# Optimization experiments

Measured on AMD Instinct MI355X. Metric: run time of the kernel, lower is better.

Reference implementation:

```python
import jax, jax.numpy as jnp
import numpy as np

N = 100000
IN_PLANES = 64
OUT_PLANES = 64
SHARE = 8
NSAMPLE = 16


def setup_inputs() -> dict:
    key = jax.random.key(0)
    ks = jax.random.split(key, 20)
    f32 = jnp.float32
    s = lambda fan_in: 1.0 / np.sqrt(fan_in)
    inp = {}
    inp['p'] = jax.random.normal(ks[0], (N, 3), f32)
    inp['x'] = jax.random.normal(ks[1], (N, IN_PLANES), f32)
    inp['knn_idx'] = jax.random.randint(ks[2], (N, NSAMPLE), 0, N, jnp.int64)
    # channelMixMLPs01: Linear(3+in, nsample) -> ReLU -> Bilinear(ns, ns, ns)
    inp['W01'] = jax.random.uniform(ks[3], (3 + IN_PLANES, NSAMPLE), f32, -s(3 + IN_PLANES), s(3 + IN_PLANES))
    inp['b01'] = jnp.zeros((NSAMPLE,), f32)
    inp['Wbil'] = jax.random.uniform(ks[4], (NSAMPLE, NSAMPLE, NSAMPLE), f32, -s(NSAMPLE), s(NSAMPLE))
    inp['bbil'] = jnp.zeros((NSAMPLE,), f32)
    # linear_p: Linear(3,3) -> BN(3) -> ReLU -> Linear(3, out)
    inp['Wp1'] = jax.random.uniform(ks[5], (3, 3), f32, -s(3), s(3))
    inp['bp1'] = jnp.zeros((3,), f32)
    inp['bnp_s'] = jnp.ones((3,), f32)   # BN folded (inference): scale = gamma/sqrt(var+eps)
    inp['bnp_b'] = jnp.zeros((3,), f32)  # shift = beta - mean*scale
    inp['Wp2'] = jax.random.uniform(ks[6], (3, OUT_PLANES), f32, -s(3), s(3))
    inp['bp2'] = jnp.zeros((OUT_PLANES,), f32)
    # channelMixMLPs02
    mid = OUT_PLANES
    inp['W2a'] = jax.random.uniform(ks[7], (2 * NSAMPLE, mid), f32, -s(2 * NSAMPLE), s(2 * NSAMPLE))
    inp['bn2a_s'] = jnp.ones((mid,), f32)
    inp['bn2a_b'] = jnp.zeros((mid,), f32)
    inp['W2b'] = jax.random.uniform(ks[8], (mid, mid // SHARE), f32, -s(mid), s(mid))
    inp['bn2b_s'] = jnp.ones((mid // SHARE,), f32)
    inp['bn2b_b'] = jnp.zeros((mid // SHARE,), f32)
    inp['W2c'] = jax.random.uniform(ks[9], (mid // SHARE, OUT_PLANES // SHARE), f32, -s(mid // SHARE), s(mid // SHARE))
    inp['b2c'] = jnp.zeros((OUT_PLANES // SHARE,), f32)
    # channelMixMLPs03: Linear(in, out)
    inp['W3'] = jax.random.uniform(ks[10], (IN_PLANES, OUT_PLANES), f32, -s(IN_PLANES), s(IN_PLANES))
    inp['b3'] = jnp.zeros((OUT_PLANES,), f32)
    return inp


def reference(p, x, knn_idx, W01, b01, Wbil, bbil, Wp1, bp1, bnp_s, bnp_b,
              Wp2, bp2, W2a, bn2a_s, bn2a_b, W2b, bn2b_s, bn2b_b, W2c, b2c,
              W3, b3):
    n, k = knn_idx.shape
    out_planes = W3.shape[1]
    share = SHARE
    # queryandgroup(use_xyz=True): gather neighbors, relative xyz concat features
    p_r = p[knn_idx] - p[:, None, :]                      # [n,k,3]
    x_knn_in = jnp.concatenate([p_r, x[knn_idx]], -1)     # [n,k,3+in]
    xf = x_knn_in.reshape(n * k, -1)
    # channelMixMLPs01: Linear -> ReLU -> Bilinear(e, e)
    e = jax.nn.relu(xf @ W01 + b01)                       # [nk, ns]
    e = jnp.einsum('ni,oij,nj->no', e, Wbil, e) + bbil    # [nk, ns]
    # linear_p on relative coords
    pe = p_r.reshape(-1, 3) @ Wp1 + bp1
    pe = jax.nn.relu(pe * bnp_s + bnp_b)
    pe = pe @ Wp2 + bp2                                   # [nk, out]
    p_embed = pe.reshape(n, k, out_planes)
    # shrink_p: (n k (a b)) -> sum over a -> (nk, b=nsample)
    a = out_planes // k
    shrink = pe.reshape(n * k, a, k).sum(1)               # [nk, ns]
    ef = jnp.concatenate([e, shrink], -1)                 # [nk, 2*ns]
    # channelMixMLPs02
    h = jax.nn.relu((ef @ W2a) * bn2a_s + bn2a_b)
    h = jax.nn.relu((h @ W2b) * bn2b_s + bn2b_b)
    h = h @ W2c + b2c                                     # [nk, out/share]
    w = jax.nn.softmax(h.reshape(n, k, -1), axis=1)       # softmax over neighbors
    # channelMixMLPs03 then gather
    x_v = (x @ W3 + b3)[knn_idx]                          # [n,k,out]
    x_knn = (x_v + p_embed).reshape(n, k, share, out_planes // share)
    x_knn = (x_knn * w[:, :, None, :]).reshape(n, k, out_planes)
    x_out = x_knn.sum(1)                                  # [n,out]
    return (x_out, x_knn, knn_idx, p_r)
```

## Files before the change

kernel.cpp:

```cpp
#include <hip/hip_runtime.h>

#define NPTS 100000
#define NK   1600000

typedef __attribute__((ext_vector_type(8))) short bf16x8;
typedef __attribute__((ext_vector_type(4))) float f32x4;
typedef union { bf16x8 v; unsigned u[4]; } fragu;

#define MFMA(a,b,c) __builtin_amdgcn_mfma_f32_16x16x32_bf16((a),(b),(c),0,0,0)

#define WS_W01  0
#define WS_WBIL 1536
#define WS_W2A  5632
#define WS_W2B  7680
#define WS_WPE  8704
#define WS_BYTES 21504
#define WS_XBF   WS_BYTES
#define WS_YBF   (WS_BYTES + 12800000)
#define WS_NEED  (WS_BYTES + 25600000)

__device__ inline unsigned cvtpk(float lo, float hi) {
  unsigned r;
  asm("v_cvt_pk_bf16_f32 %0, %1, %2" : "=v"(r) : "v"(lo), "v"(hi));
  return r;
}
__device__ inline short bfr(float f) {
  unsigned u = __float_as_uint(f);
  u += 0x7fff + ((u >> 16) & 1);
  return (short)(u >> 16);
}
__device__ inline float bflo(unsigned u) { return __uint_as_float(u << 16); }
__device__ inline float bfhi(unsigned u) { return __uint_as_float(u & 0xffff0000u); }

template<int CTRL>
__device__ inline float fdpp(float x) {
  return __int_as_float(__builtin_amdgcn_update_dpp(
      0, __float_as_int(x), CTRL, 0xF, 0xF, true));
}
template<int XM>
__device__ inline float fswz(float x) {
  return __int_as_float(__builtin_amdgcn_ds_swizzle(
      __float_as_int(x), 0x1F | (XM << 10)));
}
__device__ inline unsigned bpermu(int src, unsigned v) {
  return (unsigned)__builtin_amdgcn_ds_bpermute(src << 2, (int)v);
}
__device__ inline float bpermf(int src, float v) {
  return __int_as_float(__builtin_amdgcn_ds_bpermute(src << 2, __float_as_int(v)));
}
__device__ inline int bpermi(int src, int v) {
  return __builtin_amdgcn_ds_bpermute(src << 2, v);
}

__global__ __launch_bounds__(256) void k_pre(
    const float* __restrict__ x, const float* __restrict__ W3,
    const float* __restrict__ b3,
    const float* __restrict__ W01, const float* __restrict__ b01,
    const float* __restrict__ Wbil,
    const float* __restrict__ W2a, const float* __restrict__ W2b,
    const float* __restrict__ Wp2, const float* __restrict__ bp2,
    short* __restrict__ ws, short* __restrict__ xbf, short* __restrict__ ybf)
{
  const int b = blockIdx.x;
  if (b < 25000) {
    int t = b * 256 + threadIdx.x;
    int i = __builtin_amdgcn_readfirstlane(t >> 6);
    int c = t & 63;
    xbf[i * 64 + c] = bfr(x[i * 64 + c]);
    const float* xr = x + i * 64;
    float acc = b3[c];
#pragma unroll
    for (int k = 0; k < 64; ++k)
      acc = fmaf(xr[k], W3[k * 64 + c], acc);
    ybf[i * 64 + c] = bfr(acc);
    return;
  }
  const int t = threadIdx.x;
  for (int i = t; i < 3 * 512; i += 256) {
    int tt = i & 7, l = (i >> 3) & 63, kc = i >> 9;
    int o = l & 15, k = kc * 32 + ((l >> 4) << 3) + tt;
    float v = 0.f;
    if (k < 64) v = W01[(3 + k) * 16 + o];
    else if (k < 67) v = W01[(k - 64) * 16 + o];
    else if (k == 67) v = b01[o];
    ws[WS_W01 + i] = bfr(v);
  }
  for (int i = t; i < 8 * 512; i += 256) {
    int tt = i & 7, l = (i >> 3) & 63, kc = i >> 9;
    int o = l & 15, k = kc * 32 + ((l >> 4) << 3) + tt;
    ws[WS_WBIL + i] = bfr(Wbil[o * 256 + k]);
  }
  for (int i = t; i < 4 * 512; i += 256) {
    int tt = i & 7, l = (i >> 3) & 63, nt = i >> 9;
    int c = nt * 16 + (l & 15), k = ((l >> 4) << 3) + tt;
    ws[WS_W2A + i] = bfr(W2a[k * 64 + c]);
  }
  for (int i = t; i < 2 * 512; i += 256) {
    int tt = i & 7, l = (i >> 3) & 63, kc = i >> 9;
    int m = l & 15, k = kc * 32 + ((l >> 4) << 3) + tt;
    ws[WS_W2B + i] = bfr(m < 8 ? W2b[k * 8 + m] : 0.f);
  }
  for (int i = t; i < 4 * 512; i += 256) {
    int tt = i & 7, l = (i >> 3) & 63, nt = i >> 9;
    int c = nt * 16 + (l & 15), k = ((l >> 4) << 3) + tt;
    float v = 0.f;
    if (k < 3) v = Wp2[k * 64 + c]; else if (k == 3) v = bp2[c];
    ws[WS_WPE + i] = bfr(v);
  }
}

__global__ __launch_bounds__(256) void k_prep(
    const float* __restrict__ W01, const float* __restrict__ b01,
    const float* __restrict__ Wbil,
    const float* __restrict__ W2a, const float* __restrict__ W2b,
    const float* __restrict__ Wp2, const float* __restrict__ bp2,
    short* __restrict__ ws)
{
  const int t = threadIdx.x;
  for (int i = t; i < 3 * 512; i += 256) {
    int tt = i & 7, l = (i >> 3) & 63, kc = i >> 9;
    int o = l & 15, k = kc * 32 + ((l >> 4) << 3) + tt;
    float v = 0.f;
    if (k < 64) v = W01[(3 + k) * 16 + o];
    else if (k < 67) v = W01[(k - 64) * 16 + o];
    else if (k == 67) v = b01[o];
    ws[WS_W01 + i] = bfr(v);
  }
  for (int i = t; i < 8 * 512; i += 256) {
    int tt = i & 7, l = (i >> 3) & 63, kc = i >> 9;
    int o = l & 15, k = kc * 32 + ((l >> 4) << 3) + tt;
    ws[WS_WBIL + i] = bfr(Wbil[o * 256 + k]);
  }
  for (int i = t; i < 4 * 512; i += 256) {
    int tt = i & 7, l = (i >> 3) & 63, nt = i >> 9;
    int c = nt * 16 + (l & 15), k = ((l >> 4) << 3) + tt;
    ws[WS_W2A + i] = bfr(W2a[k * 64 + c]);
  }
  for (int i = t; i < 2 * 512; i += 256) {
    int tt = i & 7, l = (i >> 3) & 63, kc = i >> 9;
    int m = l & 15, k = kc * 32 + ((l >> 4) << 3) + tt;
    ws[WS_W2B + i] = bfr(m < 8 ? W2b[k * 8 + m] : 0.f);
  }
  for (int i = t; i < 4 * 512; i += 256) {
    int tt = i & 7, l = (i >> 3) & 63, nt = i >> 9;
    int c = nt * 16 + (l & 15), k = ((l >> 4) << 3) + tt;
    float v = 0.f;
    if (k < 3) v = Wp2[k * 64 + c]; else if (k == 3) v = bp2[c];
    ws[WS_WPE + i] = bfr(v);
  }
}

__global__ __launch_bounds__(256) void k_xw3f(
    const float* __restrict__ x, const float* __restrict__ W3,
    const float* __restrict__ b3, float* __restrict__ y)
{
  int t = blockIdx.x * 256 + threadIdx.x;
  int i = __builtin_amdgcn_readfirstlane(t >> 6);
  int c = t & 63;
  if (i >= NPTS) return;
  const float* xr = x + i * 64;
  float acc = b3[c];
#pragma unroll
  for (int k = 0; k < 64; ++k)
    acc = fmaf(xr[k], W3[k * 64 + c], acc);
  y[i * 64 + c] = acc;
}

template<bool BF>
__global__ __launch_bounds__(256, 5) void k_main(
    const float* __restrict__ p, const float* __restrict__ x,
    const int* __restrict__ knn, const short* __restrict__ wsf,
    const float* __restrict__ Wp1, const float* __restrict__ bp1,
    const float* __restrict__ bnp_s, const float* __restrict__ bnp_b,
    const float* __restrict__ bbil,
    const float* __restrict__ bn2a_s, const float* __restrict__ bn2a_b,
    const float* __restrict__ bn2b_s, const float* __restrict__ bn2b_b,
    const float* __restrict__ W2c, const float* __restrict__ b2c,
    const float* __restrict__ Wp2, const float* __restrict__ bp2,
    const void* __restrict__ yv_, const void* __restrict__ xbf_,
    float* __restrict__ x_out, float* __restrict__ x_knn,
    float* __restrict__ knn_f, float* __restrict__ p_r)
{
  const int tid  = threadIdx.x;
  const int lane = tid & 63;
  const int mloc = lane & 15;
  const int kblk = lane >> 4;
  const int row  = blockIdx.x * 256 + tid;
  const int n    = row >> 4;
  const int j    = row & 15;
  const int idx  = knn[row];

  const float pr0 = p[idx * 3 + 0] - p[n * 3 + 0];
  const float pr1 = p[idx * 3 + 1] - p[n * 3 + 1];
  const float pr2 = p[idx * 3 + 2] - p[n * 3 + 2];

  float q0, q1, q2;
  {
    float v0 = bp1[0] + pr0 * Wp1[0] + pr1 * Wp1[3] + pr2 * Wp1[6];
    float v1 = bp1[1] + pr0 * Wp1[1] + pr1 * Wp1[4] + pr2 * Wp1[7];
    float v2 = bp1[2] + pr0 * Wp1[2] + pr1 * Wp1[5] + pr2 * Wp1[8];
    q0 = fmaxf(fmaf(v0, bnp_s[0], bnp_b[0]), 0.f);
    q1 = fmaxf(fmaf(v1, bnp_s[1], bnp_b[1]), 0.f);
    q2 = fmaxf(fmaf(v2, bnp_s[2], bnp_b[2]), 0.f);
  }

#define FR(off, idx_) (((const bf16x8*)wsf)[(off) / 8 + (idx_)])

  unsigned epk[4][2];
  {
    bf16x8 bw0 = FR(WS_W01, 0 * 64 + lane);
    bf16x8 bw1 = FR(WS_W01, 1 * 64 + lane);
    bf16x8 bw2 = FR(WS_W01, 2 * 64 + lane);
    const float4* x4 = (const float4*)x;
    const bf16x8* xb8 = (const bf16x8*)xbf_;
#pragma unroll
    for (int g = 0; g < 4; ++g) {
      const int src = g * 16 + mloc;
      int   ridx = bpermi(src, idx);
      float p0s  = bpermf(src, pr0);
      float p1s  = bpermf(src, pr1);
      float p2s  = bpermf(src, pr2);
      f32x4 acc = {0.f, 0.f, 0.f, 0.f};
      if constexpr (BF) {
        bf16x8 B0 = xb8[ridx * 8 + kblk];
        bf16x8 B1 = xb8[ridx * 8 + 4 + kblk];
        acc = MFMA(bw0, B0, acc);
        acc = MFMA(bw1, B1, acc);
      } else {
        {
          float4 xa = x4[ridx * 16 + kblk * 2];
          float4 xb = x4[ridx * 16 + kblk * 2 + 1];
          fragu B;
          B.u[0] = cvtpk(xa.x, xa.y); B.u[1] = cvtpk(xa.z, xa.w);
          B.u[2] = cvtpk(xb.x, xb.y); B.u[3] = cvtpk(xb.z, xb.w);
          acc = MFMA(bw0, B.v, acc);
        }
        {
          float4 xa = x4[ridx * 16 + 8 + kblk * 2];
          float4 xb = x4[ridx * 16 + 9 + kblk * 2];
          fragu B;
          B.u[0] = cvtpk(xa.x, xa.y); B.u[1] = cvtpk(xa.z, xa.w);
          B.u[2] = cvtpk(xb.x, xb.y); B.u[3] = cvtpk(xb.z, xb.w);
          acc = MFMA(bw1, B.v, acc);
        }
      }
      {
        fragu B;
        B.u[0] = (kblk == 0) ? cvtpk(p0s, p1s) : 0u;
        B.u[1] = (kblk == 0) ? cvtpk(p2s, 1.f) : 0u;
        B.u[2] = 0u; B.u[3] = 0u;
        acc = MFMA(bw2, B.v, acc);
      }
      epk[g][0] = cvtpk(fmaxf(acc[0], 0.f), fmaxf(acc[1], 0.f));
      epk[g][1] = cvtpk(fmaxf(acc[2], 0.f), fmaxf(acc[3], 0.f));
    }
  }

  unsigned h2p[4][2];
#pragma unroll
  for (int g = 0; g < 4; ++g) {
    float er[16];
    {
      unsigned a0 = bpermu(mloc,      epk[g][0]);
      unsigned a1 = bpermu(mloc,      epk[g][1]);
      unsigned b0 = bpermu(mloc + 16, epk[g][0]);
      unsigned b1 = bpermu(mloc + 16, epk[g][1]);
      unsigned c0 = bpermu(mloc + 32, epk[g][0]);
      unsigned c1 = bpermu(mloc + 32, epk[g][1]);
      unsigned d0 = bpermu(mloc + 48, epk[g][0]);
      unsigned d1 = bpermu(mloc + 48, epk[g][1]);
      er[0] = bflo(a0);  er[1] = bfhi(a0);  er[2]  = bflo(a1); er[3]  = bfhi(a1);
      er[4] = bflo(b0);  er[5] = bfhi(b0);  er[6]  = bflo(b1); er[7]  = bfhi(b1);
      er[8] = bflo(c0);  er[9] = bfhi(c0);  er[10] = bflo(c1); er[11] = bfhi(c1);
      er[12] = bflo(d0); er[13] = bfhi(d0); er[14] = bflo(d1); er[15] = bfhi(d1);
    }
    const int jhsel = kblk & 1, ihsel = kblk >> 1;
    float ej[8];
#pragma unroll
    for (int t = 0; t < 8; ++t) ej[t] = jhsel ? er[8 + t] : er[t];
    f32x4 acc2;
    {
      f32x4 bb = *(const f32x4*)&bbil[kblk * 4];
      acc2 = bb;
#pragma unroll
      for (int kc = 0; kc < 8; ++kc) {
        bf16x8 wb = FR(WS_WBIL, kc * 64 + lane);
        float ei = ihsel ? er[2 * kc + 1] : er[2 * kc];
        fragu B;
        B.u[0] = cvtpk(ei * ej[0], ei * ej[1]);
        B.u[1] = cvtpk(ei * ej[2], ei * ej[3]);
        B.u[2] = cvtpk(ei * ej[4], ei * ej[5]);
        B.u[3] = cvtpk(ei * ej[6], ei * ej[7]);
        acc2 = MFMA(wb, B.v, acc2);
      }
    }
    f32x4 shq;
    {
      const int src = g * 16 + mloc;
      float q0s = bpermf(src, q0);
      float q1s = bpermf(src, q1);
      float q2s = bpermf(src, q2);
      fragu B;
      B.u[0] = (kblk == 0) ? cvtpk(q0s, q1s) : 0u;
      B.u[1] = (kblk == 0) ? cvtpk(q2s, 1.f) : 0u;
      B.u[2] = 0u; B.u[3] = 0u;
      f32x4 z = {0.f, 0.f, 0.f, 0.f};
      f32x4 s0 = MFMA(FR(WS_WPE, 0 * 64 + lane), B.v, z);
      f32x4 s1 = MFMA(FR(WS_WPE, 1 * 64 + lane), B.v, z);
      f32x4 s2 = MFMA(FR(WS_WPE, 2 * 64 + lane), B.v, z);
      f32x4 s3 = MFMA(FR(WS_WPE, 3 * 64 + lane), B.v, z);
#pragma unroll
      for (int r = 0; r < 4; ++r) shq[r] = s0[r] + s1[r] + s2[r] + s3[r];
    }
    unsigned pe2_0 = cvtpk(acc2[0], acc2[1]);
    unsigned pe2_1 = cvtpk(acc2[2], acc2[3]);
    unsigned psh_0 = cvtpk(shq[0], shq[1]);
    unsigned psh_1 = cvtpk(shq[2], shq[3]);
    fragu Bef;
    {
      const int s1l = mloc + 32 * (kblk & 1);
      const int s2l = s1l + 16;
      unsigned a0 = bpermu(s1l, pe2_0);
      unsigned a1 = bpermu(s1l, pe2_1);
      unsigned a2 = bpermu(s2l, pe2_0);
      unsigned a3 = bpermu(s2l, pe2_1);
      unsigned b0 = bpermu(s1l, psh_0);
      unsigned b1 = bpermu(s1l, psh_1);
      unsigned b2 = bpermu(s2l, psh_0);
      unsigned b3 = bpermu(s2l, psh_1);
      const bool lo2 = (kblk < 2);
      Bef.u[0] = lo2 ? a0 : b0; Bef.u[1] = lo2 ? a1 : b1;
      Bef.u[2] = lo2 ? a2 : b2; Bef.u[3] = lo2 ? a3 : b3;
    }
    unsigned pha[8];
#pragma unroll
    for (int nt = 0; nt < 4; ++nt) {
      bf16x8 wa = FR(WS_W2A, nt * 64 + lane);
      f32x4 z = {0.f, 0.f, 0.f, 0.f};
      f32x4 c = MFMA(wa, Bef.v, z);
      f32x4 sA = *(const f32x4*)&bn2a_s[nt * 16 + kblk * 4];
      f32x4 bA = *(const f32x4*)&bn2a_b[nt * 16 + kblk * 4];
      float h0 = fmaxf(fmaf(c[0], sA[0], bA[0]), 0.f);
      float h1 = fmaxf(fmaf(c[1], sA[1], bA[1]), 0.f);
      float h2 = fmaxf(fmaf(c[2], sA[2], bA[2]), 0.f);
      float h3 = fmaxf(fmaf(c[3], sA[3], bA[3]), 0.f);
      pha[nt * 2 + 0] = cvtpk(h0, h1);
      pha[nt * 2 + 1] = cvtpk(h2, h3);
    }
    {
      const int sAl = mloc + 32 * (kblk & 1);
      const int sBl = sAl + 16;
      const bool lo2 = (kblk < 2);
      fragu B0, B1;
      {
        unsigned a0 = bpermu(sAl, pha[0]), a1 = bpermu(sAl, pha[1]);
        unsigned a2 = bpermu(sBl, pha[0]), a3 = bpermu(sBl, pha[1]);
        unsigned b0 = bpermu(sAl, pha[2]), b1 = bpermu(sAl, pha[3]);
        unsigned b2 = bpermu(sBl, pha[2]), b3 = bpermu(sBl, pha[3]);
        B0.u[0] = lo2 ? a0 : b0; B0.u[1] = lo2 ? a1 : b1;
        B0.u[2] = lo2 ? a2 : b2; B0.u[3] = lo2 ? a3 : b3;
      }
      {
        unsigned a0 = bpermu(sAl, pha[4]), a1 = bpermu(sAl, pha[5]);
        unsigned a2 = bpermu(sBl, pha[4]), a3 = bpermu(sBl, pha[5]);
        unsigned b0 = bpermu(sAl, pha[6]), b1 = bpermu(sAl, pha[7]);
        unsigned b2 = bpermu(sBl, pha[6]), b3 = bpermu(sBl, pha[7]);
        B1.u[0] = lo2 ? a0 : b0; B1.u[1] = lo2 ? a1 : b1;
        B1.u[2] = lo2 ? a2 : b2; B1.u[3] = lo2 ? a3 : b3;
      }
      f32x4 acc3 = {0.f, 0.f, 0.f, 0.f};
      acc3 = MFMA(FR(WS_W2B, 0 * 64 + lane), B0.v, acc3);
      acc3 = MFMA(FR(WS_W2B, 1 * 64 + lane), B1.v, acc3);
      f32x4 s = *(const f32x4*)&bn2b_s[(kblk & 1) * 4];
      f32x4 b = *(const f32x4*)&bn2b_b[(kblk & 1) * 4];
      float v0 = fmaxf(fmaf(acc3[0], s[0], b[0]), 0.f);
      float v1 = fmaxf(fmaf(acc3[1], s[1], b[1]), 0.f);
      float v2 = fmaxf(fmaf(acc3[2], s[2], b[2]), 0.f);
      float v3 = fmaxf(fmaf(acc3[3], s[3], b[3]), 0.f);
      h2p[g][0] = cvtpk(v0, v1);
      h2p[g][1] = cvtpk(v2, v3);
    }
  }

  unsigned hp0 = 0, hp1 = 0, hp2 = 0, hp3 = 0;
#pragma unroll
  for (int g = 0; g < 4; ++g) {
    unsigned t0 = bpermu(mloc,      h2p[g][0]);
    unsigned t1 = bpermu(mloc,      h2p[g][1]);
    unsigned t2 = bpermu(mloc + 16, h2p[g][0]);
    unsigned t3 = bpermu(mloc + 16, h2p[g][1]);
    const bool mine = (kblk == g);
    hp0 = mine ? t0 : hp0; hp1 = mine ? t1 : hp1;
    hp2 = mine ? t2 : hp2; hp3 = mine ? t3 : hp3;
  }
  float h2r[8];
  h2r[0] = bflo(hp0); h2r[1] = bfhi(hp0); h2r[2] = bflo(hp1); h2r[3] = bfhi(hp1);
  h2r[4] = bflo(hp2); h2r[5] = bfhi(hp2); h2r[6] = bflo(hp3); h2r[7] = bfhi(hp3);

  float h3[8];
#pragma unroll
  for (int b = 0; b < 8; ++b) h3[b] = b2c[b];
#pragma unroll
  for (int m = 0; m < 8; ++m) {
    float r = h2r[m];
#pragma unroll
    for (int b = 0; b < 8; ++b) h3[b] = fmaf(r, W2c[m * 8 + b], h3[b]);
  }
  float wv[8];
#pragma unroll
  for (int b = 0; b < 8; ++b) {
    float mx = h3[b];
    mx = fmaxf(mx, fdpp<0x128>(mx));
    mx = fmaxf(mx, fdpp<0x124>(mx));
    mx = fmaxf(mx, fdpp<0x122>(mx));
    mx = fmaxf(mx, fdpp<0x121>(mx));
    float ex = __expf(h3[b] - mx);
    float s = ex;
    s = s + fdpp<0x128>(s);
    s = s + fdpp<0x124>(s);
    s = s + fdpp<0x122>(s);
    s = s + fdpp<0x121>(s);
    wv[b] = ex * __builtin_amdgcn_rcpf(s);
  }

  float* xkrow = x_knn + (long long)row * 64;
  float xo[4];
#pragma unroll
  for (int h = 0; h < 2; ++h) {
    float v[32];
    if constexpr (BF) {
      const uint4* y4b = (const uint4*)yv_;
#pragma unroll
      for (int u2 = 0; u2 < 4; ++u2) {
        uint4 yw = y4b[idx * 8 + h * 4 + u2];
        unsigned wd[4] = {yw.x, yw.y, yw.z, yw.w};
#pragma unroll
        for (int half = 0; half < 2; ++half) {
          const int u = u2 * 2 + half;
          float comp[4] = {bflo(wd[half * 2]), bfhi(wd[half * 2]),
                           bflo(wd[half * 2 + 1]), bfhi(wd[half * 2 + 1])};
          f32x4 st;
#pragma unroll
          for (int cc = 0; cc < 4; ++cc) {
            const int c = h * 32 + u * 4 + cc;
            float pe = bp2[c] + q0 * Wp2[c] + q1 * Wp2[64 + c] + q2 * Wp2[128 + c];
            float val = (comp[cc] + pe) * wv[c & 7];
            v[u * 4 + cc] = val;
            st[cc] = val;
          }
          *(f32x4*)(xkrow + h * 32 + u * 4) = st;
        }
      }
    } else {
      const float4* y4 = (const float4*)yv_;
#pragma unroll
      for (int u = 0; u < 8; ++u) {
        float4 yw = y4[idx * 16 + h * 8 + u];
        float comp[4] = {yw.x, yw.y, yw.z, yw.w};
        f32x4 st;
#pragma unroll
        for (int cc = 0; cc < 4; ++cc) {
          const int c = h * 32 + u * 4 + cc;
          float pe = bp2[c] + q0 * Wp2[c] + q1 * Wp2[64 + c] + q2 * Wp2[128 + c];
          float val = (comp[cc] + pe) * wv[c & 7];
          v[u * 4 + cc] = val;
          st[cc] = val;
        }
        *(f32x4*)(xkrow + h * 32 + u * 4) = st;
      }
    }
    const bool b0 = (j & 1), b1 = (j & 2), b2 = (j & 4), b3 = (j & 8);
    float v1[16];
#pragma unroll
    for (int q = 0; q < 16; ++q) {
      float snd = b0 ? v[2 * q] : v[2 * q + 1];
      float rcv = fdpp<0xB1>(snd);
      v1[q] = (b0 ? v[2 * q + 1] : v[2 * q]) + rcv;
    }
    float v2[8];
#pragma unroll
    for (int r = 0; r < 8; ++r) {
      float snd = b1 ? v1[2 * r] : v1[2 * r + 1];
      float rcv = fdpp<0x4E>(snd);
      v2[r] = (b1 ? v1[2 * r + 1] : v1[2 * r]) + rcv;
    }
    float v3[4];
#pragma unroll
    for (int s = 0; s < 4; ++s) {
      float snd = b2 ? v2[2 * s] : v2[2 * s + 1];
      float rcv = fswz<4>(snd);
      v3[s] = (b2 ? v2[2 * s + 1] : v2[2 * s]) + rcv;
    }
    {
      float s0 = b3 ? v3[0] : v3[1];
      float s1 = b3 ? v3[2] : v3[3];
      float r0 = fswz<8>(s0);
      float r1 = fswz<8>(s1);
      xo[2 * h]     = (b3 ? v3[1] : v3[0]) + r0;
      xo[2 * h + 1] = (b3 ? v3[3] : v3[2]) + r1;
    }
  }
#pragma unroll
  for (int g = 0; g < 4; ++g)
    x_out[n * 64 + g * 16 + j] = xo[g];

  if (knn_f) {
    knn_f[row] = (float)idx;
    p_r[row * 3 + 0] = pr0;
    p_r[row * 3 + 1] = pr1;
    p_r[row * 3 + 2] = pr2;
  }
}

__global__ __launch_bounds__(256) void k_tail(
    const float* __restrict__ p, const int* __restrict__ knn,
    float* __restrict__ knn_f, float* __restrict__ p_r)
{
  int row = blockIdx.x * 256 + threadIdx.x;
  if (row >= NK) return;
  int n = row >> 4;
  int idx = knn[row];
  knn_f[row] = (float)idx;
  p_r[row * 3 + 0] = p[idx * 3 + 0] - p[n * 3 + 0];
  p_r[row * 3 + 1] = p[idx * 3 + 1] - p[n * 3 + 1];
  p_r[row * 3 + 2] = p[idx * 3 + 2] - p[n * 3 + 2];
}

extern "C" void kernel_launch(void* const* d_in, const int* in_sizes, int n_in,
                              void* d_out, int out_size, void* d_ws, size_t ws_size,
                              hipStream_t stream)
{
  const float* p    = (const float*)d_in[0];
  const float* x    = (const float*)d_in[1];
  const int*   knn  = (const int*)d_in[2];
  const float* W01  = (const float*)d_in[3];
  const float* b01  = (const float*)d_in[4];
  const float* Wbil = (const float*)d_in[5];
  const float* bbil = (const float*)d_in[6];
  const float* Wp1  = (const float*)d_in[7];
  const float* bp1  = (const float*)d_in[8];
  const float* bnps = (const float*)d_in[9];
  const float* bnpb = (const float*)d_in[10];
  const float* Wp2  = (const float*)d_in[11];
  const float* bp2  = (const float*)d_in[12];
  const float* W2a  = (const float*)d_in[13];
  const float* s2a  = (const float*)d_in[14];
  const float* b2a  = (const float*)d_in[15];
  const float* W2b  = (const float*)d_in[16];
  const float* s2b  = (const float*)d_in[17];
  const float* b2b  = (const float*)d_in[18];
  const float* W2c  = (const float*)d_in[19];
  const float* b2c  = (const float*)d_in[20];
  const float* W3   = (const float*)d_in[21];
  const float* b3   = (const float*)d_in[22];

  float* outF  = (float*)d_out;
  float* x_out = outF;
  float* x_knn = outF + 6400000;
  float* knn_f = outF + 108800000;
  float* p_r   = outF + 110400000;
  short* wsf   = (short*)d_ws;

  if (ws_size >= (size_t)WS_NEED) {
    short* xbf = (short*)((char*)d_ws + WS_XBF);
    short* ybf = (short*)((char*)d_ws + WS_YBF);
    k_pre<<<25001, 256, 0, stream>>>(x, W3, b3, W01, b01, Wbil, W2a, W2b,
                                     Wp2, bp2, wsf, xbf, ybf);
    k_main<true><<<6250, 256, 0, stream>>>(p, x, knn, wsf, Wp1, bp1, bnps, bnpb,
                                           bbil, s2a, b2a, s2b, b2b, W2c, b2c,
                                           Wp2, bp2, ybf, xbf, x_out, x_knn,
                                           knn_f, p_r);
  } else {
    float* y = knn_f;
    k_prep<<<1, 256, 0, stream>>>(W01, b01, Wbil, W2a, W2b, Wp2, bp2, wsf);
    k_xw3f<<<25000, 256, 0, stream>>>(x, W3, b3, y);
    k_main<false><<<6250, 256, 0, stream>>>(p, x, knn, wsf, Wp1, bp1, bnps, bnpb,
                                            bbil, s2a, b2a, s2b, b2b, W2c, b2c,
                                            Wp2, bp2, y, nullptr, x_out, x_knn,
                                            (float*)nullptr, (float*)nullptr);
    k_tail<<<6250, 256, 0, stream>>>(p, knn, knn_f, p_r);
  }
}
```

Baseline: 362.3 us.

## Precompute per-point x@W01 projection before gathering neighbors

The first Linear layer is split by linearity: the x-part (x@W01[3:]) is computed once per point in the pre-kernel and stored as 16 bf16 values. The main kernel then gathers 32 bytes per neighbor instead of a 128-byte bf16 row of x, and adds the 3-coordinate term and bias with scalar FMAs instead of running MFMAs. This cuts gather traffic and matrix work in the main kernel. The cost is an extra 64-length dot product for 16 of the 64 channels in the pre-kernel, plus rounding the projection to bf16 before the bias is added.

```diff
diff --git a/kernel.cpp b/kernel.cpp
--- a/kernel.cpp
+++ b/kernel.cpp
@@ -15,9 +15,9 @@
 #define WS_W2B  7680
 #define WS_WPE  8704
 #define WS_BYTES 21504
-#define WS_XBF   WS_BYTES
-#define WS_YBF   (WS_BYTES + 12800000)
-#define WS_NEED  (WS_BYTES + 25600000)
+#define WS_EX    WS_BYTES
+#define WS_YBF   (WS_BYTES + 3200000)
+#define WS_NEED  (WS_BYTES + 3200000 + 12800000)
 
 __device__ inline unsigned cvtpk(float lo, float hi) {
   unsigned r;
@@ -59,20 +59,26 @@
     const float* __restrict__ Wbil,
     const float* __restrict__ W2a, const float* __restrict__ W2b,
     const float* __restrict__ Wp2, const float* __restrict__ bp2,
-    short* __restrict__ ws, short* __restrict__ xbf, short* __restrict__ ybf)
+    short* __restrict__ ws, short* __restrict__ exbf, short* __restrict__ ybf)
 {
   const int b = blockIdx.x;
   if (b < 25000) {
     int t = b * 256 + threadIdx.x;
     int i = __builtin_amdgcn_readfirstlane(t >> 6);
     int c = t & 63;
-    xbf[i * 64 + c] = bfr(x[i * 64 + c]);
     const float* xr = x + i * 64;
     float acc = b3[c];
 #pragma unroll
     for (int k = 0; k < 64; ++k)
       acc = fmaf(xr[k], W3[k * 64 + c], acc);
     ybf[i * 64 + c] = bfr(acc);
+    if (c < 16) {
+      float a2 = 0.f;
+#pragma unroll
+      for (int k = 0; k < 64; ++k)
+        a2 = fmaf(xr[k], W01[(3 + k) * 16 + c], a2);
+      exbf[i * 16 + c] = bfr(a2);
+    }
     return;
   }
   const int t = threadIdx.x;
@@ -170,6 +176,7 @@
 __global__ __launch_bounds__(256, 5) void k_main(
     const float* __restrict__ p, const float* __restrict__ x,
     const int* __restrict__ knn, const short* __restrict__ wsf,
+    const float* __restrict__ W01, const float* __restrict__ b01,
     const float* __restrict__ Wp1, const float* __restrict__ bp1,
     const float* __restrict__ bnp_s, const float* __restrict__ bnp_b,
     const float* __restrict__ bbil,
@@ -177,7 +184,7 @@
     const float* __restrict__ bn2b_s, const float* __restrict__ bn2b_b,
     const float* __restrict__ W2c, const float* __restrict__ b2c,
     const float* __restrict__ Wp2, const float* __restrict__ bp2,
-    const void* __restrict__ yv_, const void* __restrict__ xbf_,
+    const void* __restrict__ yv_, const void* __restrict__ exbf_,
     float* __restrict__ x_out, float* __restrict__ x_knn,
     float* __restrict__ knn_f, float* __restrict__ p_r)
 {
@@ -207,12 +214,36 @@
 #define FR(off, idx_) (((const bf16x8*)wsf)[(off) / 8 + (idx_)])
 
   unsigned epk[4][2];
-  {
+  if constexpr (BF) {
+    f32x4 w0 = *(const f32x4*)&W01[ 0 + kblk * 4];
+    f32x4 w1 = *(const f32x4*)&W01[16 + kblk * 4];
+    f32x4 w2 = *(const f32x4*)&W01[32 + kblk * 4];
+    f32x4 bb = *(const f32x4*)&b01[kblk * 4];
+    const unsigned* ex2 = (const unsigned*)exbf_;
+#pragma unroll
+    for (int g = 0; g < 4; ++g) {
+      const int src = g * 16 + mloc;
+      int   ridx = bpermi(src, idx);
+      float p0s  = bpermf(src, pr0);
+      float p1s  = bpermf(src, pr1);
+      float p2s  = bpermf(src, pr2);
+      uint2 exw = *(const uint2*)&ex2[ridx * 8 + kblk * 2];
+      float e0 = bflo(exw.x) + bb[0];
+      float e1 = bfhi(exw.x) + bb[1];
+      float e2 = bflo(exw.y) + bb[2];
+      float e3 = bfhi(exw.y) + bb[3];
+      e0 = fmaf(p0s, w0[0], e0); e0 = fmaf(p1s, w1[0], e0); e0 = fmaf(p2s, w2[0], e0);
+      e1 = fmaf(p0s, w0[1], e1); e1 = fmaf(p1s, w1[1], e1); e1 = fmaf(p2s, w2[1], e1);
+      e2 = fmaf(p0s, w0[2], e2); e2 = fmaf(p1s, w1[2], e2); e2 = fmaf(p2s, w2[2], e2);
+      e3 = fmaf(p0s, w0[3], e3); e3 = fmaf(p1s, w1[3], e3); e3 = fmaf(p2s, w2[3], e3);
+      epk[g][0] = cvtpk(fmaxf(e0, 0.f), fmaxf(e1, 0.f));
+      epk[g][1] = cvtpk(fmaxf(e2, 0.f), fmaxf(e3, 0.f));
+    }
+  } else {
     bf16x8 bw0 = FR(WS_W01, 0 * 64 + lane);
     bf16x8 bw1 = FR(WS_W01, 1 * 64 + lane);
     bf16x8 bw2 = FR(WS_W01, 2 * 64 + lane);
     const float4* x4 = (const float4*)x;
-    const bf16x8* xb8 = (const bf16x8*)xbf_;
 #pragma unroll
     for (int g = 0; g < 4; ++g) {
       const int src = g * 16 + mloc;
@@ -221,28 +252,21 @@
       float p1s  = bpermf(src, pr1);
       float p2s  = bpermf(src, pr2);
       f32x4 acc = {0.f, 0.f, 0.f, 0.f};
-      if constexpr (BF) {
-        bf16x8 B0 = xb8[ridx * 8 + kblk];
-        bf16x8 B1 = xb8[ridx * 8 + 4 + kblk];
-        acc = MFMA(bw0, B0, acc);
-        acc = MFMA(bw1, B1, acc);
-      } else {
-        {
-          float4 xa = x4[ridx * 16 + kblk * 2];
-          float4 xb = x4[ridx * 16 + kblk * 2 + 1];
-          fragu B;
-          B.u[0] = cvtpk(xa.x, xa.y); B.u[1] = cvtpk(xa.z, xa.w);
-          B.u[2] = cvtpk(xb.x, xb.y); B.u[3] = cvtpk(xb.z, xb.w);
-          acc = MFMA(bw0, B.v, acc);
-        }
-        {
-          float4 xa = x4[ridx * 16 + 8 + kblk * 2];
-          float4 xb = x4[ridx * 16 + 9 + kblk * 2];
-          fragu B;
-          B.u[0] = cvtpk(xa.x, xa.y); B.u[1] = cvtpk(xa.z, xa.w);
-          B.u[2] = cvtpk(xb.x, xb.y); B.u[3] = cvtpk(xb.z, xb.w);
-          acc = MFMA(bw1, B.v, acc);
-        }
+      {
+        float4 xa = x4[ridx * 16 + kblk * 2];
+        float4 xb = x4[ridx * 16 + kblk * 2 + 1];
+        fragu B;
+        B.u[0] = cvtpk(xa.x, xa.y); B.u[1] = cvtpk(xa.z, xa.w);
+        B.u[2] = cvtpk(xb.x, xb.y); B.u[3] = cvtpk(xb.z, xb.w);
+        acc = MFMA(bw0, B.v, acc);
+      }
+      {
+        float4 xa = x4[ridx * 16 + 8 + kblk * 2];
+        float4 xb = x4[ridx * 16 + 9 + kblk * 2];
+        fragu B;
+        B.u[0] = cvtpk(xa.x, xa.y); B.u[1] = cvtpk(xa.z, xa.w);
+        B.u[2] = cvtpk(xb.x, xb.y); B.u[3] = cvtpk(xb.z, xb.w);
+        acc = MFMA(bw1, B.v, acc);
       }
       {
         fragu B;
@@ -562,19 +586,21 @@
   short* wsf   = (short*)d_ws;
 
   if (ws_size >= (size_t)WS_NEED) {
-    short* xbf = (short*)((char*)d_ws + WS_XBF);
-    short* ybf = (short*)((char*)d_ws + WS_YBF);
+    short* exbf = (short*)((char*)d_ws + WS_EX);
+    short* ybf  = (short*)((char*)d_ws + WS_YBF);
     k_pre<<<25001, 256, 0, stream>>>(x, W3, b3, W01, b01, Wbil, W2a, W2b,
-                                     Wp2, bp2, wsf, xbf, ybf);
-    k_main<true><<<6250, 256, 0, stream>>>(p, x, knn, wsf, Wp1, bp1, bnps, bnpb,
+                                     Wp2, bp2, wsf, exbf, ybf);
+    k_main<true><<<6250, 256, 0, stream>>>(p, x, knn, wsf, W01, b01,
+                                           Wp1, bp1, bnps, bnpb,
                                            bbil, s2a, b2a, s2b, b2b, W2c, b2c,
-                                           Wp2, bp2, ybf, xbf, x_out, x_knn,
+                                           Wp2, bp2, ybf, exbf, x_out, x_knn,
                                            knn_f, p_r);
   } else {
     float* y = knn_f;
     k_prep<<<1, 256, 0, stream>>>(W01, b01, Wbil, W2a, W2b, Wp2, bp2, wsf);
     k_xw3f<<<25000, 256, 0, stream>>>(x, W3, b3, y);
-    k_main<false><<<6250, 256, 0, stream>>>(p, x, knn, wsf, Wp1, bp1, bnps, bnpb,
+    k_main<false><<<6250, 256, 0, stream>>>(p, x, knn, wsf, W01, b01,
+                                            Wp1, bp1, bnps, bnpb,
                                             bbil, s2a, b2a, s2b, b2b, W2c, b2c,
                                             Wp2, bp2, y, nullptr, x_out, x_knn,
                                             (float*)nullptr, (float*)nullptr);
```

Result: slower. 390.3 us (+7.7%).
